# Kernel tuning notes

Measured on AMD Instinct MI355X. Metric: run time of the kernel, lower is better.

The kernel has to match this reference:

```python
import jax, jax.numpy as jnp
import numpy as np

DIM = 2048
N_HEADS = 16
N_KV_HEADS = 4
HEAD_DIM = 128
EPS = 1e-6
BS, SEQ = 2, 4096


def setup_inputs() -> dict:
    key = jax.random.key(0)
    ks = jax.random.split(key, 8)
    x = jax.random.normal(ks[0], (BS, SEQ, DIM), dtype=jnp.float32)
    # rotary freqs: unit-modulus complex represented as [seq, head_dim//2, 2]
    theta = 10000.0
    inv_freq = 1.0 / (theta ** (jnp.arange(0, HEAD_DIM, 2, dtype=jnp.float32) / HEAD_DIM))
    t = jnp.arange(SEQ, dtype=jnp.float32)
    ang = jnp.outer(t, inv_freq)  # [SEQ, HEAD_DIM//2]
    freqs_cis = jnp.stack([jnp.cos(ang), jnp.sin(ang)], axis=-1)  # [SEQ, HD/2, 2]
    std = 0.02
    wq = jax.random.normal(ks[1], (N_HEADS * HEAD_DIM, DIM), dtype=jnp.float32) * std
    wk = jax.random.normal(ks[2], (N_KV_HEADS * HEAD_DIM, DIM), dtype=jnp.float32) * std
    wv = jax.random.normal(ks[3], (N_KV_HEADS * HEAD_DIM, DIM), dtype=jnp.float32) * std
    wo = jax.random.normal(ks[4], (DIM, N_HEADS * HEAD_DIM), dtype=jnp.float32) * std
    q_norm_w = jnp.ones((HEAD_DIM,), dtype=jnp.float32)
    k_norm_w = jnp.ones((HEAD_DIM,), dtype=jnp.float32)
    return {"x": x, "freqs_cis": freqs_cis, "wq": wq, "wk": wk, "wv": wv,
            "wo": wo, "q_norm_w": q_norm_w, "k_norm_w": k_norm_w}


def _rms_norm(x, w, eps=EPS):
    xf = x.astype(jnp.float32)
    var = jnp.mean(xf * xf, axis=-1, keepdims=True)
    return w * (xf * jax.lax.rsqrt(var + eps)).astype(x.dtype)


def _apply_rope(x, freqs_cis):
    # x: [b, s, h, d]; freqs_cis: [s, d//2, 2] (cos, sin)
    b, s, h, d = x.shape
    xr = x.astype(jnp.float32).reshape(b, s, h, d // 2, 2)
    cos = freqs_cis[:s, :, 0][None, :, None, :]
    sin = freqs_cis[:s, :, 1][None, :, None, :]
    xre, xim = xr[..., 0], xr[..., 1]
    out = jnp.stack([xre * cos - xim * sin, xre * sin + xim * cos], axis=-1)
    return out.reshape(b, s, h, d).astype(x.dtype)


def reference(x, freqs_cis, wq, wk, wv, wo, q_norm_w, k_norm_w):
    bs, seqlen, _ = x.shape
    xq = jnp.einsum('bsd,ed->bse', x, wq).reshape(bs, seqlen, N_HEADS, HEAD_DIM)
    xk = jnp.einsum('bsd,ed->bse', x, wk).reshape(bs, seqlen, N_KV_HEADS, HEAD_DIM)
    xv = jnp.einsum('bsd,ed->bse', x, wv).reshape(bs, seqlen, N_KV_HEADS, HEAD_DIM)
    xq = _rms_norm(xq, q_norm_w)
    xk = _rms_norm(xk, k_norm_w)
    xq = _apply_rope(xq, freqs_cis)
    xk = _apply_rope(xk, freqs_cis)
    n_rep = N_HEADS // N_KV_HEADS
    # repeat_kv: [b,s,kvh,d] -> [b,s,kvh*n_rep,d]
    keys = jnp.repeat(xk, n_rep, axis=2)
    values = jnp.repeat(xv, n_rep, axis=2)
    q = xq.transpose(0, 2, 1, 3)  # [b,h,s,d]
    k = keys.transpose(0, 2, 1, 3)
    v = values.transpose(0, 2, 1, 3)
    scale = 1.0 / jnp.sqrt(jnp.asarray(HEAD_DIM, dtype=q.dtype))
    scores = jnp.einsum('bhqd,bhkd->bhqk', q, k) * scale
    causal = jnp.tril(jnp.ones((seqlen, seqlen), dtype=bool))
    scores = jnp.where(causal[None, None], scores, jnp.finfo(scores.dtype).min)
    attn = jax.nn.softmax(scores, axis=-1)
    out = jnp.einsum('bhqk,bhkd->bhqd', attn, v)
    out = out.transpose(0, 2, 1, 3).reshape(bs, seqlen, N_HEADS * HEAD_DIM)
    return jnp.einsum('bse,de->bsd', out, wo)
```

## Files before the change

kernel.cpp:

```cpp
#include <hip/hip_runtime.h>

typedef __bf16 bf16;
typedef __bf16 bf16x8 __attribute__((ext_vector_type(8)));
typedef __bf16 bf16x4 __attribute__((ext_vector_type(4)));
typedef __bf16 bf16x2 __attribute__((ext_vector_type(2)));
typedef float  f32x4  __attribute__((ext_vector_type(4)));

static_assert(sizeof(bf16x8) == 16, "bf16x8 must be 16B");

#define MFMA16(a, b, c) __builtin_amdgcn_mfma_f32_16x16x32_bf16((a), (b), (c), 0, 0, 0)

__device__ __forceinline__ void gload_lds16(const void* g, void* l) {
    __builtin_amdgcn_global_load_lds(
        (const __attribute__((address_space(1))) void*)(uintptr_t)g,
        (__attribute__((address_space(3))) void*)(uintptr_t)l,
        16, 0, 0);
}

__global__ __launch_bounds__(256)
void cast_f32_bf16(const float* __restrict__ in, bf16* __restrict__ out, int n8)
{
    const int i = blockIdx.x * 256 + threadIdx.x;
    if (i >= n8) return;
    const float4 a = ((const float4*)in)[i * 2];
    const float4 b = ((const float4*)in)[i * 2 + 1];
    bf16x8 o;
    o[0] = (bf16)a.x; o[1] = (bf16)a.y; o[2] = (bf16)a.z; o[3] = (bf16)a.w;
    o[4] = (bf16)b.x; o[5] = (bf16)b.y; o[6] = (bf16)b.z; o[7] = (bf16)b.w;
    ((bf16x8*)out)[i] = o;
}

template <typename OT>
__global__ __launch_bounds__(256)
void gemm_bt(const bf16* __restrict__ A, const bf16* __restrict__ W,
             int K, int ldc, OT* __restrict__ C)
{
    __shared__ bf16 As[128 * 64];
    __shared__ bf16 Bs[128 * 64];

    const int n0 = blockIdx.x * 128;
    const int m0 = blockIdx.y * 128;

    const int tid  = threadIdx.x;
    const int lane = tid & 63;
    const int wid  = tid >> 6;
    const int wm   = wid >> 1;
    const int wn   = wid & 1;
    const int quad = lane >> 4;
    const int l16  = lane & 15;
    const int key  = l16 & 7;

    const int srow  = wid * 32 + (lane >> 3);
    const int scolg = ((lane & 7) ^ (lane >> 3)) * 8;
    const bf16* ag = A + (size_t)(m0 + srow) * K + scolg;
    const bf16* wg = W + (size_t)(n0 + srow) * K + scolg;
    bf16* al = As + wid * 2048;
    bf16* bl = Bs + wid * 2048;

    f32x4 acc[4][4];
#pragma unroll
    for (int i = 0; i < 4; i++)
#pragma unroll
        for (int j = 0; j < 4; j++) acc[i][j] = f32x4{0.f, 0.f, 0.f, 0.f};

    for (int kt = 0; kt < K; kt += 64) {
        __syncthreads();
#pragma unroll
        for (int i = 0; i < 4; i++) {
            gload_lds16(ag + (size_t)(i * 8) * K, al + i * 8 * 64);
            gload_lds16(wg + (size_t)(i * 8) * K, bl + i * 8 * 64);
        }
        ag += 64; wg += 64;
        __syncthreads();

#pragma unroll
        for (int ks = 0; ks < 2; ks++) {
            bf16x8 af[4], bfv[4];
#pragma unroll
            for (int i = 0; i < 4; i++)
                af[i]  = *(const bf16x8*)(As + (wm * 64 + i * 16 + l16) * 64 + (((ks * 4 + quad) ^ key) * 8));
#pragma unroll
            for (int i = 0; i < 4; i++)
                bfv[i] = *(const bf16x8*)(Bs + (wn * 64 + i * 16 + l16) * 64 + (((ks * 4 + quad) ^ key) * 8));
#pragma unroll
            for (int mi = 0; mi < 4; mi++)
#pragma unroll
                for (int ni = 0; ni < 4; ni++)
                    acc[mi][ni] = MFMA16(af[mi], bfv[ni], acc[mi][ni]);
        }
    }

#pragma unroll
    for (int mi = 0; mi < 4; mi++) {
        const int row = m0 + wm * 64 + mi * 16 + quad * 4;
#pragma unroll
        for (int ni = 0; ni < 4; ni++) {
            const int col = n0 + wn * 64 + ni * 16 + l16;
#pragma unroll
            for (int r = 0; r < 4; r++)
                C[(size_t)(row + r) * ldc + col] = (OT)acc[mi][ni][r];
        }
    }
}

__global__ __launch_bounds__(256)
void normrope(bf16* __restrict__ qkv, const float* __restrict__ fc,
              const float* __restrict__ qw, const float* __restrict__ kw)
{
    const int row  = blockIdx.x * 4 + (threadIdx.x >> 6);
    const int lane = threadIdx.x & 63;
    const int slot = row % 20;
    const int tok  = row / 20;
    const int s    = tok & 4095;

    const float* w; int off; float post;
    if (slot < 16) { off = slot * 128;               w = qw; post = 0.12751681555f; }
    else           { off = 2048 + (slot - 16) * 128; w = kw; post = 1.0f; }

    bf16* p = qkv + (size_t)tok * 3072 + off;

    bf16x2 v = *(const bf16x2*)(p + 2 * lane);
    float x0 = (float)v[0], x1 = (float)v[1];

    float ss = x0 * x0 + x1 * x1;
    ss += __shfl_xor(ss, 1);  ss += __shfl_xor(ss, 2);  ss += __shfl_xor(ss, 4);
    ss += __shfl_xor(ss, 8);  ss += __shfl_xor(ss, 16); ss += __shfl_xor(ss, 32);
    const float r = rsqrtf(ss * (1.0f / 128.0f) + 1e-6f) * post;

    const float xn0 = x0 * r * w[2 * lane], xn1 = x1 * r * w[2 * lane + 1];

    const float2 cs = ((const float2*)fc)[(size_t)s * 64 + lane];
    const float c = cs.x, sn = cs.y;

    bf16x2 o;
    o[0] = (bf16)(xn0 * c - xn1 * sn);
    o[1] = (bf16)(xn0 * sn + xn1 * c);
    *(bf16x2*)(p + 2 * lane) = o;
}

__global__ __launch_bounds__(256)
void transpose_v(const bf16* __restrict__ qkv, bf16* __restrict__ vT)
{
    __shared__ bf16 T[64][130];
    const int st = blockIdx.x;
    const int bk = blockIdx.y;
    const int b = bk >> 2, kvh = bk & 3;
    const int w = threadIdx.x >> 6, lane = threadIdx.x & 63;
    const int s0 = st * 64;

    const bf16* src = qkv + (size_t)(b * 4096 + s0) * 3072 + 2560 + kvh * 128;
#pragma unroll
    for (int i = 0; i < 16; i++) {
        const int s = w * 16 + i;
        const bf16x2 v = *(const bf16x2*)(src + (size_t)s * 3072 + 2 * lane);
        *(bf16x2*)(&T[s][2 * lane]) = v;
    }
    __syncthreads();

    bf16* dst = vT + ((size_t)bk * 128) * 4096 + s0;
#pragma unroll
    for (int i = 0; i < 16; i++) {
        const int d = w * 32 + 2 * i + (lane >> 5);
        const int s = (lane & 31) * 2;
        bf16x2 o;
        o[0] = T[s][d];
        o[1] = T[s + 1][d];
        *(bf16x2*)(dst + (size_t)d * 4096 + s) = o;
    }
}

__global__ __launch_bounds__(256, 2)
void flash(const bf16* __restrict__ qkv, const bf16* __restrict__ vT,
           bf16* __restrict__ out)
{
    const int bh  = blockIdx.y;
    const int b   = bh >> 4, h = bh & 15;
    const int kvh = h >> 2;

    const int tid  = threadIdx.x;
    const int lane = tid & 63;
    const int wid  = tid >> 6;
    const int quad = lane >> 4;
    const int l16  = lane & 15;
    const int key  = l16 & 7;

    __shared__ bf16 Ks[2][64 * 128];
    __shared__ bf16 Vs[128 * 64];
    __shared__ bf16 Ps[128 * 64];

    const bf16* kbase = qkv + (size_t)b * 4096 * 3072 + 2048 + kvh * 128;
    const bf16* vbase = vT + ((size_t)(b * 4 + kvh) * 128) * 4096;

    const int krow_off = lane >> 4;
    const int kcolg    = lane & 15;
    const int vrow_off = lane >> 3;
    const int vcolg    = lane & 7;

    for (int pass = 0; pass < 2; ++pass) {
        const int qt = pass ? (31 - blockIdx.x) : blockIdx.x;
        const int q0 = qt * 128;
        const int ntiles = qt * 2 + 2;

        __syncthreads();
#pragma unroll
        for (int i = 0; i < 4; i++) {
            const int r0 = wid * 16 + i * 4;
            const int rk = r0 + krow_off;
            const int gc = (kcolg ^ (rk & 7)) * 8;
            gload_lds16(kbase + (size_t)rk * 3072 + gc, &Ks[0][r0 * 128]);
        }

        bf16x8 qf[2][4];
        const bf16* qbase = qkv + ((size_t)(b * 4096 + q0 + wid * 32)) * 3072 + h * 128;
#pragma unroll
        for (int mt = 0; mt < 2; mt++)
#pragma unroll
            for (int ks = 0; ks < 4; ks++)
                qf[mt][ks] = *(const bf16x8*)(qbase + (size_t)(mt * 16 + l16) * 3072 + ks * 32 + quad * 8);

        f32x4 oacc[2][8];
#pragma unroll
        for (int mt = 0; mt < 2; mt++)
#pragma unroll
            for (int nd = 0; nd < 8; nd++) oacc[mt][nd] = f32x4{0.f, 0.f, 0.f, 0.f};
        float mrow[2], lrow[2];
#pragma unroll
        for (int mt = 0; mt < 2; mt++) { mrow[mt] = -__builtin_inff(); lrow[mt] = 0.f; }

        __syncthreads();

#pragma unroll
        for (int i = 0; i < 4; i++) {
            const int r0 = wid * 32 + i * 8;
            const int dv = r0 + vrow_off;
            const int gc = (vcolg ^ (dv & 7)) * 8;
            gload_lds16(vbase + (size_t)dv * 4096 + gc, &Vs[r0 * 64]);
        }
#pragma unroll
        for (int i = 0; i < 4; i++) {
            const int r0 = wid * 16 + i * 4;
            const int rk = r0 + krow_off;
            const int gc = (kcolg ^ (rk & 7)) * 8;
            gload_lds16(kbase + (size_t)(64 + rk) * 3072 + gc, &Ks[1][r0 * 128]);
        }

        f32x4 sA[2][4], sB[2][4];

        {
#pragma unroll
            for (int mt = 0; mt < 2; mt++)
#pragma unroll
                for (int nt = 0; nt < 4; nt++) sA[mt][nt] = f32x4{0.f, 0.f, 0.f, 0.f};
            __builtin_amdgcn_s_setprio(1);
#pragma unroll
            for (int ks = 0; ks < 4; ks++) {
                bf16x8 kf[4];
#pragma unroll
                for (int nt = 0; nt < 4; nt++)
                    kf[nt] = *(const bf16x8*)(&Ks[0][(nt * 16 + l16) * 128 + (((ks * 4 + quad) ^ key) * 8)]);
#pragma unroll
                for (int mt = 0; mt < 2; mt++)
#pragma unroll
                    for (int nt = 0; nt < 4; nt++)
                        sA[mt][nt] = MFMA16(kf[nt], qf[mt][ks], sA[mt][nt]);
            }
            __builtin_amdgcn_s_setprio(0);
        }

        auto step = [&](int t, f32x4 (&SA)[2][4], f32x4 (&SB)[2][4]) {
            const int kv0 = t * 64;

            if (kv0 + 63 > q0) {
#pragma unroll
                for (int mt = 0; mt < 2; mt++) {
                    const int qg = q0 + wid * 32 + mt * 16 + l16;
#pragma unroll
                    for (int nt = 0; nt < 4; nt++)
#pragma unroll
                        for (int r = 0; r < 4; r++) {
                            const int kvg = kv0 + nt * 16 + quad * 4 + r;
                            if (kvg > qg) SA[mt][nt][r] = -1e30f;
                        }
                }
            }

            float pm[2];
#pragma unroll
            for (int mt = 0; mt < 2; mt++) {
                float t8[8];
#pragma unroll
                for (int nt = 0; nt < 4; nt++) {
                    t8[2 * nt]     = fmaxf(SA[mt][nt][0], SA[mt][nt][1]);
                    t8[2 * nt + 1] = fmaxf(SA[mt][nt][2], SA[mt][nt][3]);
                }
                float m = fmaxf(fmaxf(fmaxf(t8[0], t8[1]), fmaxf(t8[2], t8[3])),
                                fmaxf(fmaxf(t8[4], t8[5]), fmaxf(t8[6], t8[7])));
                m = fmaxf(m, __shfl_xor(m, 16));
                m = fmaxf(m, __shfl_xor(m, 32));
                pm[mt] = m;
            }

            const bool rescale =
                !__all((pm[0] - mrow[0] <= 8.f) && (pm[1] - mrow[1] <= 8.f));
            if (rescale) {
#pragma unroll
                for (int mt = 0; mt < 2; mt++) {
                    const float mnew  = fmaxf(mrow[mt], pm[mt]);
                    const float alpha = exp2f(mrow[mt] - mnew);
                    mrow[mt] = mnew;
                    lrow[mt] *= alpha;
                    float ar[4];
#pragma unroll
                    for (int r = 0; r < 4; r++) ar[r] = __shfl(alpha, quad * 4 + r);
#pragma unroll
                    for (int nd = 0; nd < 8; nd++)
#pragma unroll
                        for (int r = 0; r < 4; r++) oacc[mt][nd][r] *= ar[r];
                }
            }

#pragma unroll
            for (int mt = 0; mt < 2; mt++) {
                const int prow = wid * 32 + mt * 16 + l16;
                float sn[4];
#pragma unroll
                for (int nt = 0; nt < 4; nt++) {
                    const float p0 = exp2f(SA[mt][nt][0] - mrow[mt]);
                    const float p1 = exp2f(SA[mt][nt][1] - mrow[mt]);
                    const float p2 = exp2f(SA[mt][nt][2] - mrow[mt]);
                    const float p3 = exp2f(SA[mt][nt][3] - mrow[mt]);
                    sn[nt] = (p0 + p1) + (p2 + p3);
                    bf16x4 h4;
                    h4[0] = (bf16)p0; h4[1] = (bf16)p1;
                    h4[2] = (bf16)p2; h4[3] = (bf16)p3;
                    const int g = (2 * nt + (quad >> 1)) ^ key;
                    *(bf16x4*)(&Ps[prow * 64 + g * 8 + (quad & 1) * 4]) = h4;
                }
                float s = (sn[0] + sn[1]) + (sn[2] + sn[3]);
                s += __shfl_xor(s, 16);
                s += __shfl_xor(s, 32);
                lrow[mt] += s;
            }

            __syncthreads();

            if (t + 1 < ntiles) {
#pragma unroll
                for (int mt = 0; mt < 2; mt++)
#pragma unroll
                    for (int nt = 0; nt < 4; nt++) SB[mt][nt] = f32x4{0.f, 0.f, 0.f, 0.f};
                __builtin_amdgcn_s_setprio(1);
#pragma unroll
                for (int ks = 0; ks < 4; ks++) {
                    bf16x8 kf[4];
#pragma unroll
                    for (int nt = 0; nt < 4; nt++)
                        kf[nt] = *(const bf16x8*)(&Ks[(t + 1) & 1][(nt * 16 + l16) * 128 + (((ks * 4 + quad) ^ key) * 8)]);
#pragma unroll
                    for (int mt = 0; mt < 2; mt++)
#pragma unroll
                        for (int nt = 0; nt < 4; nt++)
                            SB[mt][nt] = MFMA16(kf[nt], qf[mt][ks], SB[mt][nt]);
                }
                __builtin_amdgcn_s_setprio(0);
            }

            __builtin_amdgcn_s_setprio(1);
#pragma unroll
            for (int ks = 0; ks < 2; ks++) {
                bf16x8 pf[2];
#pragma unroll
                for (int mt = 0; mt < 2; mt++)
                    pf[mt] = *(const bf16x8*)(&Ps[(wid * 32 + mt * 16 + l16) * 64 + (((ks * 4 + quad) ^ key) * 8)]);
#pragma unroll
                for (int nd = 0; nd < 8; nd++) {
                    const bf16x8 vf = *(const bf16x8*)(&Vs[(nd * 16 + l16) * 64 + (((ks * 4 + quad) ^ key) * 8)]);
#pragma unroll
                    for (int mt = 0; mt < 2; mt++)
                        oacc[mt][nd] = MFMA16(pf[mt], vf, oacc[mt][nd]);
                }
            }
            __builtin_amdgcn_s_setprio(0);

            if (t + 1 < ntiles) {
                __syncthreads();
                const int kvv = (t + 1) * 64;
#pragma unroll
                for (int i = 0; i < 4; i++) {
                    const int r0 = wid * 32 + i * 8;
                    const int dv = r0 + vrow_off;
                    const int gc = (vcolg ^ (dv & 7)) * 8;
                    gload_lds16(vbase + (size_t)dv * 4096 + kvv + gc, &Vs[r0 * 64]);
                }
                if (t + 2 < ntiles) {
                    const int kvn = (t + 2) * 64;
#pragma unroll
                    for (int i = 0; i < 4; i++) {
                        const int r0 = wid * 16 + i * 4;
                        const int rk = r0 + krow_off;
                        const int gc = (kcolg ^ (rk & 7)) * 8;
                        gload_lds16(kbase + (size_t)(kvn + rk) * 3072 + gc, &Ks[t & 1][r0 * 128]);
                    }
                }
            }
        };

        for (int t = 0; t < ntiles; t += 2) {
            step(t,     sA, sB);
            step(t + 1, sB, sA);
        }

#pragma unroll
        for (int mt = 0; mt < 2; mt++) {
            const float inv = 1.0f / lrow[mt];
            float invr[4];
#pragma unroll
            for (int r = 0; r < 4; r++) invr[r] = __shfl(inv, quad * 4 + r);
#pragma unroll
            for (int r = 0; r < 4; r++) {
                const size_t srow = (size_t)(b * 4096 + q0 + wid * 32 + mt * 16 + quad * 4 + r);
#pragma unroll
                for (int nd = 0; nd < 8; nd++)
                    out[srow * 2048 + h * 128 + nd * 16 + l16] = (bf16)(oacc[mt][nd][r] * invr[r]);
            }
        }
    }
}

extern "C" void kernel_launch(void* const* d_in, const int* in_sizes, int n_in,
                              void* d_out, int out_size, void* d_ws, size_t ws_size,
                              hipStream_t stream)
{
    const float* x   = (const float*)d_in[0];
    const float* fc  = (const float*)d_in[1];
    const float* wq  = (const float*)d_in[2];
    const float* wk  = (const float*)d_in[3];
    const float* wv  = (const float*)d_in[4];
    const float* wo  = (const float*)d_in[5];
    const float* qnw = (const float*)d_in[6];
    const float* knw = (const float*)d_in[7];
    float* out = (float*)d_out;

    char* ws = (char*)d_ws;
    bf16* qkv = (bf16*)ws;
    bf16* vT  = (bf16*)(ws + 50331648);
    bf16* xb  = (bf16*)(ws + 58720256);
    bf16* att = xb;
    bf16* wb  = (bf16*)(ws + 92274688);
    bf16* wob = wb;

    cast_f32_bf16<<<dim3(8192), 256, 0, stream>>>(x, xb, 2097152);
    cast_f32_bf16<<<dim3(2048), 256, 0, stream>>>(wq, wb, 524288);
    cast_f32_bf16<<<dim3(512),  256, 0, stream>>>(wk, wb + 2048 * 2048, 131072);
    cast_f32_bf16<<<dim3(512),  256, 0, stream>>>(wv, wb + 2560 * 2048, 131072);
    gemm_bt<bf16><<<dim3(24, 64), 256, 0, stream>>>(xb, wb, 2048, 3072, qkv);
    normrope<<<dim3(40960), 256, 0, stream>>>(qkv, fc, qnw, knw);
    transpose_v<<<dim3(64, 8), 256, 0, stream>>>(qkv, vT);
    flash<<<dim3(16, 32), 256, 0, stream>>>(qkv, vT, att);
    cast_f32_bf16<<<dim3(2048), 256, 0, stream>>>(wo, wob, 524288);
    gemm_bt<float><<<dim3(16, 64), 256, 0, stream>>>(att, wob, 2048, 2048, out);
}
```

Before: 632.9 us.

## Fuse casts into one launch, V transpose into QKV GEMM epilogue, wo cast into normrope

Merges the four input/weight cast kernels into a single launch and folds the wo cast into the norm+rope kernel as extra blocks. The QKV GEMM epilogue now writes V tiles transposed through swizzled shared memory directly into vT, eliminating the separate transpose kernel and its extra read/write of V. This cuts kernel launches and memory traffic at the cost of a more branchy GEMM epilogue; V is no longer written to the qkv buffer.

```diff
diff --git a/kernel.cpp b/kernel.cpp
--- a/kernel.cpp
+++ b/kernel.cpp
@@ -17,11 +17,8 @@
         16, 0, 0);
 }
 
-__global__ __launch_bounds__(256)
-void cast_f32_bf16(const float* __restrict__ in, bf16* __restrict__ out, int n8)
-{
-    const int i = blockIdx.x * 256 + threadIdx.x;
-    if (i >= n8) return;
+__device__ __forceinline__ void cast8(const float* __restrict__ in, bf16* __restrict__ out, int i)
+{
     const float4 a = ((const float4*)in)[i * 2];
     const float4 b = ((const float4*)in)[i * 2 + 1];
     bf16x8 o;
@@ -30,13 +27,31 @@
     ((bf16x8*)out)[i] = o;
 }
 
-template <typename OT>
+__global__ __launch_bounds__(256)
+void cast_all(const float* __restrict__ x,  const float* __restrict__ wq,
+              const float* __restrict__ wk, const float* __restrict__ wv,
+              bf16* __restrict__ xb, bf16* __restrict__ wb)
+{
+    const int blk = blockIdx.x;
+    if (blk < 8192) {
+        cast8(x, xb, blk * 256 + threadIdx.x);
+    } else if (blk < 10240) {
+        cast8(wq, wb, (blk - 8192) * 256 + threadIdx.x);
+    } else if (blk < 10752) {
+        cast8(wk, wb + 2048 * 2048, (blk - 10240) * 256 + threadIdx.x);
+    } else {
+        cast8(wv, wb + 2560 * 2048, (blk - 10752) * 256 + threadIdx.x);
+    }
+}
+
+template <typename OT, bool FUSE_VT>
 __global__ __launch_bounds__(256)
 void gemm_bt(const bf16* __restrict__ A, const bf16* __restrict__ W,
-             int K, int ldc, OT* __restrict__ C)
-{
-    __shared__ bf16 As[128 * 64];
-    __shared__ bf16 Bs[128 * 64];
+             int K, int ldc, OT* __restrict__ C, bf16* __restrict__ vTp)
+{
+    __shared__ bf16 smem[2 * 128 * 64];
+    bf16* As = smem;
+    bf16* Bs = smem + 128 * 64;
 
     const int n0 = blockIdx.x * 128;
     const int m0 = blockIdx.y * 128;
@@ -90,6 +105,36 @@
         }
     }
 
+    if (FUSE_VT && n0 >= 2560) {
+        __syncthreads();
+        bf16* T = smem;
+#pragma unroll
+        for (int mi = 0; mi < 4; mi++) {
+            const int scol = wm * 64 + mi * 16 + quad * 4;
+            const int g    = scol >> 3;
+            const int sub  = scol & 7;
+#pragma unroll
+            for (int ni = 0; ni < 4; ni++) {
+                const int d = wn * 64 + ni * 16 + l16;
+                bf16x4 h4;
+                h4[0] = (bf16)acc[mi][ni][0]; h4[1] = (bf16)acc[mi][ni][1];
+                h4[2] = (bf16)acc[mi][ni][2]; h4[3] = (bf16)acc[mi][ni][3];
+                *(bf16x4*)(&T[d * 128 + ((g ^ (d & 7)) * 8 + sub)]) = h4;
+            }
+        }
+        __syncthreads();
+        const int kvh = (n0 - 2560) >> 7;
+        const int bb  = m0 >> 12;
+        bf16* vdst = vTp + ((size_t)((bb * 4 + kvh) * 128)) * 4096 + (m0 & 4095);
+#pragma unroll
+        for (int i = 0; i < 8; i++) {
+            const int d = wid * 32 + i * 4 + quad;
+            const bf16x8 v = *(const bf16x8*)(&T[d * 128 + ((l16 ^ (d & 7)) * 8)]);
+            *(bf16x8*)(vdst + (size_t)d * 4096 + l16 * 8) = v;
+        }
+        return;
+    }
+
 #pragma unroll
     for (int mi = 0; mi < 4; mi++) {
         const int row = m0 + wm * 64 + mi * 16 + quad * 4;
@@ -104,9 +149,14 @@
 }
 
 __global__ __launch_bounds__(256)
-void normrope(bf16* __restrict__ qkv, const float* __restrict__ fc,
-              const float* __restrict__ qw, const float* __restrict__ kw)
-{
+void normrope_wo(bf16* __restrict__ qkv, const float* __restrict__ fc,
+                 const float* __restrict__ qw, const float* __restrict__ kw,
+                 const float* __restrict__ wo, bf16* __restrict__ wob)
+{
+    if (blockIdx.x >= 40960) {
+        cast8(wo, wob, (blockIdx.x - 40960) * 256 + threadIdx.x);
+        return;
+    }
     const int row  = blockIdx.x * 4 + (threadIdx.x >> 6);
     const int lane = threadIdx.x & 63;
     const int slot = row % 20;
@@ -136,37 +186,6 @@
     o[0] = (bf16)(xn0 * c - xn1 * sn);
     o[1] = (bf16)(xn0 * sn + xn1 * c);
     *(bf16x2*)(p + 2 * lane) = o;
-}
-
-__global__ __launch_bounds__(256)
-void transpose_v(const bf16* __restrict__ qkv, bf16* __restrict__ vT)
-{
-    __shared__ bf16 T[64][130];
-    const int st = blockIdx.x;
-    const int bk = blockIdx.y;
-    const int b = bk >> 2, kvh = bk & 3;
-    const int w = threadIdx.x >> 6, lane = threadIdx.x & 63;
-    const int s0 = st * 64;
-
-    const bf16* src = qkv + (size_t)(b * 4096 + s0) * 3072 + 2560 + kvh * 128;
-#pragma unroll
-    for (int i = 0; i < 16; i++) {
-        const int s = w * 16 + i;
-        const bf16x2 v = *(const bf16x2*)(src + (size_t)s * 3072 + 2 * lane);
-        *(bf16x2*)(&T[s][2 * lane]) = v;
-    }
-    __syncthreads();
-
-    bf16* dst = vT + ((size_t)bk * 128) * 4096 + s0;
-#pragma unroll
-    for (int i = 0; i < 16; i++) {
-        const int d = w * 32 + 2 * i + (lane >> 5);
-        const int s = (lane & 31) * 2;
-        bf16x2 o;
-        o[0] = T[s][d];
-        o[1] = T[s + 1][d];
-        *(bf16x2*)(dst + (size_t)d * 4096 + s) = o;
-    }
 }
 
 __global__ __launch_bounds__(256, 2)
@@ -449,14 +468,9 @@
     bf16* wb  = (bf16*)(ws + 92274688);
     bf16* wob = wb;
 
-    cast_f32_bf16<<<dim3(8192), 256, 0, stream>>>(x, xb, 2097152);
-    cast_f32_bf16<<<dim3(2048), 256, 0, stream>>>(wq, wb, 524288);
-    cast_f32_bf16<<<dim3(512),  256, 0, stream>>>(wk, wb + 2048 * 2048, 131072);
-    cast_f32_bf16<<<dim3(512),  256, 0, stream>>>(wv, wb + 2560 * 2048, 131072);
-    gemm_bt<bf16><<<dim3(24, 64), 256, 0, stream>>>(xb, wb, 2048, 3072, qkv);
-    normrope<<<dim3(40960), 256, 0, stream>>>(qkv, fc, qnw, knw);
-    transpose_v<<<dim3(64, 8), 256, 0, stream>>>(qkv, vT);
+    cast_all<<<dim3(11264), 256, 0, stream>>>(x, wq, wk, wv, xb, wb);
+    gemm_bt<bf16, true><<<dim3(24, 64), 256, 0, stream>>>(xb, wb, 2048, 3072, qkv, vT);
+    normrope_wo<<<dim3(43008), 256, 0, stream>>>(qkv, fc, qnw, knw, wo, wob);
     flash<<<dim3(16, 32), 256, 0, stream>>>(qkv, vT, att);
-    cast_f32_bf16<<<dim3(2048), 256, 0, stream>>>(wo, wob, 524288);
-    gemm_bt<float><<<dim3(16, 64), 256, 0, stream>>>(att, wob, 2048, 2048, out);
-}
+    gemm_bt<float, false><<<dim3(16, 64), 256, 0, stream>>>(att, wob, 2048, 2048, out, nullptr);
+}
```

Result: no change. 635.8 us (+0.5%).
